# Optimization experiments

Measured on AMD Instinct MI355X. Metric: run time of the kernel, lower is better.

Reference implementation:

```python
import jax, jax.numpy as jnp
import numpy as np

N = 100000

def _gcn_layer(x, W, b, src, dst, norm):
    # dense transform then sparse normalized aggregation (scatter-add)
    h = x @ W                                  # [N, out]
    msg = h[src] * norm[:, None]               # [E+N, out]
    agg = jax.ops.segment_sum(msg, dst, num_segments=N)
    return agg + b


def setup_inputs() -> dict:
    key = jax.random.key(0)
    ks = jax.random.split(key, 12)
    num_features, hidden, num_classes = 128, 128, 32
    E = 3200000
    x = jax.random.normal(ks[0], (N, num_features), dtype=jnp.float32)
    edge_index = jax.random.randint(ks[1], (2, E), 0, N, dtype=jnp.int64)

    def glorot(k, fan_in, fan_out):
        s = (6.0 / (fan_in + fan_out)) ** 0.5
        return jax.random.uniform(k, (fan_in, fan_out), jnp.float32, -s, s)

    return {
        "x": x,
        "edge_index": edge_index,
        "W1": glorot(ks[2], num_features, hidden), "b1": jnp.zeros((hidden,), jnp.float32),
        "W2": glorot(ks[3], hidden, hidden),       "b2": jnp.zeros((hidden,), jnp.float32),
        "W3": glorot(ks[4], hidden, hidden),       "b3": jnp.zeros((hidden,), jnp.float32),
        "W4": glorot(ks[5], hidden, num_classes),  "b4": jnp.zeros((num_classes,), jnp.float32),
    }


def reference(x, edge_index, W1, b1, W2, b2, W3, b3, W4, b4):
    # GCNConv semantics: add self-loops, symmetric degree normalization
    loop = jnp.arange(N, dtype=edge_index.dtype)
    src = jnp.concatenate([edge_index[0], loop])   # [E+N]
    dst = jnp.concatenate([edge_index[1], loop])   # [E+N]
    deg = jax.ops.segment_sum(jnp.ones_like(dst, dtype=x.dtype), dst, num_segments=N)
    dinv = jnp.where(deg > 0, deg ** -0.5, 0.0)
    norm = dinv[src] * dinv[dst]                   # [E+N]

    h = _gcn_layer(x, W1, b1, src, dst, norm)
    h = jax.nn.relu(h)                              # dropout: eval mode -> identity
    h = _gcn_layer(h, W2, b2, src, dst, norm)
    h = jax.nn.relu(h)
    h = _gcn_layer(h, W3, b3, src, dst, norm)
    h = jax.nn.relu(h)
    h = _gcn_layer(h, W4, b4, src, dst, norm)
    return jax.nn.log_softmax(h, axis=1)
```

## Files before the change

### kernel.cpp

```cpp
#include <hip/hip_runtime.h>
#include <hip/hip_bf16.h>
#include <math.h>

#define NNODES 100000
#define NBMAX 512
#define CH 8192

typedef __hip_bfloat16 bf16;
typedef __attribute__((ext_vector_type(8))) short short8;
typedef __attribute__((ext_vector_type(4))) float f32x4;
typedef __attribute__((ext_vector_type(2))) float f32x2;

__device__ inline unsigned pack_bf16x2(float a, float b) {
    __hip_bfloat162 p;
    p.x = __float2bfloat16(a);
    p.y = __float2bfloat16(b);
    return *(unsigned*)&p;
}

__device__ inline float2 unpack_bf16x2(unsigned u) {
    __hip_bfloat162 p = *(__hip_bfloat162*)&u;
    return make_float2(__bfloat162float(p.x), __bfloat162float(p.y));
}

__device__ inline unsigned char f32_to_fp8(float v) {
    int p = __builtin_amdgcn_cvt_pk_fp8_f32(v, v, 0, false);
    return (unsigned char)(p & 0xff);
}

__global__ __launch_bounds__(256) void prep_w_all(const float* __restrict__ W1, bf16* __restrict__ wt1,
                                                  const float* __restrict__ W2, bf16* __restrict__ wt2,
                                                  const float* __restrict__ W3, bf16* __restrict__ wt3,
                                                  const float* __restrict__ W4, bf16* __restrict__ wt4,
                                                  int* __restrict__ bcount, int* __restrict__ done,
                                                  unsigned* __restrict__ zrow) {
    int b = blockIdx.x, t = threadIdx.x;
    if (b == 0) {
        for (int i = t; i < NBMAX; i += 256) bcount[i] = 0;
        if (t == 0) *done = 0;
        if (t < 32) zrow[t] = 0u;
    }
    const float* W; bf16* WT; int Nout, idx0;
    if (b < 64)       { W = W1; WT = wt1; Nout = 128; idx0 = b * 256; }
    else if (b < 128) { W = W2; WT = wt2; Nout = 128; idx0 = (b - 64) * 256; }
    else if (b < 192) { W = W3; WT = wt3; Nout = 128; idx0 = (b - 128) * 256; }
    else              { W = W4; WT = wt4; Nout = 32;  idx0 = (b - 192) * 256; }
    int idx = idx0 + t;
    if (idx < 128 * Nout) {
        int nn = idx >> 7;
        int kk = idx & 127;
        WT[idx] = __float2bfloat16(W[kk * Nout + nn]);
    }
}

__global__ __launch_bounds__(256) void bucket_hist_scan(const int* __restrict__ dst,
                                                        int* __restrict__ bcount,
                                                        int* __restrict__ boff,
                                                        int* __restrict__ bcursor,
                                                        int* __restrict__ done,
                                                        int E, int nb, int nblocks) {
    __shared__ int hist[NBMAX];
    __shared__ int ticket_s;
    __shared__ int wsum[4];
    int t = threadIdx.x;
    for (int i = t; i < NBMAX; i += 256) hist[i] = 0;
    __syncthreads();
    int e0 = blockIdx.x * CH;
#pragma unroll
    for (int k = 0; k < 32; ++k) {
        int e = e0 + t + k * 256;
        if (e < E) atomicAdd(&hist[dst[e] >> 8], 1);
    }
    __syncthreads();
    for (int i = t; i < nb; i += 256)
        if (hist[i]) atomicAdd(&bcount[i], hist[i]);
    __threadfence();
    __syncthreads();
    if (t == 0) ticket_s = atomicAdd(done, 1);
    __syncthreads();
    if (ticket_s != nblocks - 1) return;
    __threadfence();
    int i0 = t * 2, i1v = t * 2 + 1;
    int a  = (i0  < nb) ? atomicAdd(&bcount[i0], 0) : 0;
    int bb = (i1v < nb) ? atomicAdd(&bcount[i1v], 0) : 0;
    int v = a + bb;
    int lane = t & 63, wv = t >> 6;
    int incl = v;
#pragma unroll
    for (int dd = 1; dd < 64; dd <<= 1) {
        int x = __shfl_up(incl, dd, 64);
        if (lane >= dd) incl += x;
    }
    if (lane == 63) wsum[wv] = incl;
    __syncthreads();
    int wo = 0;
    for (int k = 0; k < wv; ++k) wo += wsum[k];
    int excl = wo + incl - v;
    if (i0 <= nb)  { boff[i0]  = excl;     if (i0  < nb) bcursor[i0]  = excl; }
    if (i1v <= nb) { boff[i1v] = excl + a; if (i1v < nb) bcursor[i1v] = excl + a; }
}

__global__ __launch_bounds__(256) void partition(const int* __restrict__ src,
                                                 const int* __restrict__ dst,
                                                 int* __restrict__ bcursor,
                                                 int* __restrict__ part, int E, int nb) {
    __shared__ int hist[NBMAX];
    __shared__ int cursor[NBMAX];
    int t = threadIdx.x;
    int e0 = blockIdx.x * CH;
    for (int i = t; i < NBMAX; i += 256) hist[i] = 0;
    __syncthreads();
    int mys[32], myd[32];
#pragma unroll
    for (int k = 0; k < 32; ++k) {
        int e = e0 + t + k * 256;
        int s = 0, dd = -1;
        if (e < E) { s = src[e]; dd = dst[e]; }
        mys[k] = s; myd[k] = dd;
        if (dd >= 0) atomicAdd(&hist[dd >> 8], 1);
    }
    __syncthreads();
    for (int i = t; i < nb; i += 256) {
        int c = hist[i];
        cursor[i] = c ? atomicAdd(&bcursor[i], c) : 0;
    }
    __syncthreads();
#pragma unroll
    for (int k = 0; k < 32; ++k) {
        int dd = myd[k];
        if (dd >= 0) {
            int lpos = atomicAdd(&cursor[dd >> 8], 1);
            part[lpos] = mys[k] | ((dd & 255) << 24);
        }
    }
}

__global__ __launch_bounds__(256) void nodes_fill(const int* __restrict__ part,
                                                  const int* __restrict__ boff,
                                                  float* __restrict__ dinv,
                                                  int2* __restrict__ off2,
                                                  int* __restrict__ edges, int n) {
    __shared__ int ndeg[256];
    __shared__ int ws2[4];
    __shared__ int offl[256];
    int b = blockIdx.x;
    int t = threadIdx.x;
    ndeg[t] = 0;
    __syncthreads();
    int r0 = boff[b], r1 = boff[b + 1];
    for (int i = r0 + t; i < r1; i += 256)
        atomicAdd(&ndeg[((unsigned)part[i]) >> 24], 1);
    __syncthreads();
    int deg = ndeg[t];
    int node = b * 256 + t;
    int lane = t & 63, wv = t >> 6;
    int incl = deg;
#pragma unroll
    for (int d = 1; d < 64; d <<= 1) {
        int x = __shfl_up(incl, d, 64);
        if (lane >= d) incl += x;
    }
    if (lane == 63) ws2[wv] = incl;
    __syncthreads();
    int wo = 0;
    for (int k = 0; k < wv; ++k) wo += ws2[k];
    int node_off = r0 + wo + incl - deg;
    if (node < n) {
        off2[node] = make_int2(node_off, node_off + deg);
        dinv[node] = rsqrtf((float)(deg + 1));
    }
    offl[t] = node_off;
    ndeg[t] = 0;
    __syncthreads();
    for (int i = r0 + t; i < r1; i += 256) {
        int rec = part[i];
        int dloc = ((unsigned)rec) >> 24;
        int lpos = atomicAdd(&ndeg[dloc], 1);
        edges[offl[dloc] + lpos] = rec & 0xFFFFFF;
    }
}

#define WSTRIDE 136

__global__ __launch_bounds__(256) void gemm128_f32A(const float* __restrict__ A,
                                                    const bf16* __restrict__ WT,
                                                    const float* __restrict__ dinv,
                                                    unsigned char* __restrict__ C, int n) {
    __shared__ bf16 wl[128 * WSTRIDE];
    int t = threadIdx.x;
#pragma unroll
    for (int l = 0; l < 8; ++l) {
        int chunk = t + l * 256;
        int row = chunk >> 4, ch = chunk & 15;
        *(uint4*)&wl[row * WSTRIDE + ch * 8] = *(const uint4*)&WT[row * 128 + ch * 8];
    }
    __syncthreads();
    int wave = t >> 6, lane = t & 63;
    int m = lane & 15, q = lane >> 4;
    int row_base = blockIdx.x * 128 + wave * 32;
    int r0 = min(row_base + m, n - 1);
    int r1 = min(row_base + 16 + m, n - 1);

    f32x4 acc[2][8];
#pragma unroll
    for (int g = 0; g < 2; ++g)
#pragma unroll
        for (int c = 0; c < 8; ++c) acc[g][c] = (f32x4)(0.f);

#pragma unroll
    for (int kt = 0; kt < 4; ++kt) {
        short8 af[2];
#pragma unroll
        for (int g = 0; g < 2; ++g) {
            const float* ap = &A[(size_t)(g ? r1 : r0) * 128 + kt * 32 + q * 8];
            float4 f0 = *(const float4*)ap;
            float4 f1 = *(const float4*)(ap + 4);
            union { uint4 u; short8 s; } cv;
            cv.u.x = pack_bf16x2(f0.x, f0.y);
            cv.u.y = pack_bf16x2(f0.z, f0.w);
            cv.u.z = pack_bf16x2(f1.x, f1.y);
            cv.u.w = pack_bf16x2(f1.z, f1.w);
            af[g] = cv.s;
        }
#pragma unroll
        for (int c = 0; c < 8; ++c) {
            short8 bf = *(const short8*)&wl[(c * 16 + m) * WSTRIDE + kt * 32 + q * 8];
            acc[0][c] = __builtin_amdgcn_mfma_f32_16x16x32_bf16(af[0], bf, acc[0][c], 0, 0, 0);
            acc[1][c] = __builtin_amdgcn_mfma_f32_16x16x32_bf16(af[1], bf, acc[1][c], 0, 0, 0);
        }
    }
    float dv[2][4];
#pragma unroll
    for (int g = 0; g < 2; ++g)
#pragma unroll
        for (int r = 0; r < 4; ++r) {
            int row = row_base + g * 16 + q * 4 + r;
            dv[g][r] = (row < n) ? dinv[row] : 0.f;
        }
#pragma unroll
    for (int g = 0; g < 2; ++g)
#pragma unroll
        for (int c = 0; c < 8; ++c)
#pragma unroll
            for (int r = 0; r < 4; ++r) {
                int row = row_base + g * 16 + q * 4 + r;
                if (row < n) C[(size_t)row * 128 + c * 16 + m] = f32_to_fp8(acc[g][c][r] * dv[g][r]);
            }
}

__global__ __launch_bounds__(256) void gemm128_bf16A(const bf16* __restrict__ A,
                                                     const bf16* __restrict__ WT,
                                                     const float* __restrict__ dinv,
                                                     unsigned char* __restrict__ C, int n) {
    __shared__ bf16 wl[128 * WSTRIDE];
    int t = threadIdx.x;
#pragma unroll
    for (int l = 0; l < 8; ++l) {
        int chunk = t + l * 256;
        int row = chunk >> 4, ch = chunk & 15;
        *(uint4*)&wl[row * WSTRIDE + ch * 8] = *(const uint4*)&WT[row * 128 + ch * 8];
    }
    __syncthreads();
    int wave = t >> 6, lane = t & 63;
    int m = lane & 15, q = lane >> 4;
    int row_base = blockIdx.x * 128 + wave * 32;
    int r0 = min(row_base + m, n - 1);
    int r1 = min(row_base + 16 + m, n - 1);

    f32x4 acc[2][8];
#pragma unroll
    for (int g = 0; g < 2; ++g)
#pragma unroll
        for (int c = 0; c < 8; ++c) acc[g][c] = (f32x4)(0.f);

#pragma unroll
    for (int kt = 0; kt < 4; ++kt) {
        short8 a0 = *(const short8*)&A[(size_t)r0 * 128 + kt * 32 + q * 8];
        short8 a1 = *(const short8*)&A[(size_t)r1 * 128 + kt * 32 + q * 8];
#pragma unroll
        for (int c = 0; c < 8; ++c) {
            short8 bf = *(const short8*)&wl[(c * 16 + m) * WSTRIDE + kt * 32 + q * 8];
            acc[0][c] = __builtin_amdgcn_mfma_f32_16x16x32_bf16(a0, bf, acc[0][c], 0, 0, 0);
            acc[1][c] = __builtin_amdgcn_mfma_f32_16x16x32_bf16(a1, bf, acc[1][c], 0, 0, 0);
        }
    }
    float dv[2][4];
#pragma unroll
    for (int g = 0; g < 2; ++g)
#pragma unroll
        for (int r = 0; r < 4; ++r) {
            int row = row_base + g * 16 + q * 4 + r;
            dv[g][r] = (row < n) ? dinv[row] : 0.f;
        }
#pragma unroll
    for (int g = 0; g < 2; ++g)
#pragma unroll
        for (int c = 0; c < 8; ++c)
#pragma unroll
            for (int r = 0; r < 4; ++r) {
                int row = row_base + g * 16 + q * 4 + r;
                if (row < n) C[(size_t)row * 128 + c * 16 + m] = f32_to_fp8(acc[g][c][r] * dv[g][r]);
            }
}

__global__ __launch_bounds__(256) void gemm32_bf16A(const bf16* __restrict__ A,
                                                    const bf16* __restrict__ WT,
                                                    const float* __restrict__ dinv,
                                                    bf16* __restrict__ C, int n) {
    if (blockIdx.x == 0 && threadIdx.x < 32)
        C[(size_t)n * 32 + threadIdx.x] = __float2bfloat16(0.f);
    int wave = threadIdx.x >> 6;
    int lane = threadIdx.x & 63;
    int m = lane & 15;
    int q = lane >> 4;
    int row_base = blockIdx.x * 64 + wave * 16;
    int arow = min(row_base + m, n - 1);

    f32x4 acc[2];
    acc[0] = (f32x4)(0.f);
    acc[1] = (f32x4)(0.f);

#pragma unroll
    for (int kt = 0; kt < 4; ++kt) {
        short8 af = *(const short8*)&A[(size_t)arow * 128 + kt * 32 + q * 8];
#pragma unroll
        for (int c = 0; c < 2; ++c) {
            short8 bf = *(const short8*)&WT[(size_t)(c * 16 + m) * 128 + kt * 32 + q * 8];
            acc[c] = __builtin_amdgcn_mfma_f32_16x16x32_bf16(af, bf, acc[c], 0, 0, 0);
        }
    }
    float dv[4];
#pragma unroll
    for (int r = 0; r < 4; ++r) {
        int row = row_base + q * 4 + r;
        dv[r] = (row < n) ? dinv[row] : 0.f;
    }
#pragma unroll
    for (int c = 0; c < 2; ++c)
#pragma unroll
        for (int r = 0; r < 4; ++r) {
            int row = row_base + q * 4 + r;
            if (row < n) C[(size_t)row * 32 + c * 16 + m] = __float2bfloat16(acc[c][r] * dv[r]);
        }
}

__global__ __launch_bounds__(256) void agg128(const unsigned char* __restrict__ h,
                                              const int2* __restrict__ off2,
                                              const int* __restrict__ edges,
                                              const float* __restrict__ dinv,
                                              const float* __restrict__ bias,
                                              bf16* __restrict__ out, int n) {
    int wid = (blockIdx.x * blockDim.x + threadIdx.x) >> 6;
    if (wid >= n) return;
    int lane = threadIdx.x & 63;
    int g = lane >> 4;
    int d = lane & 15;
    int l32 = lane & 31;
    const char* hb = (const char*)h;
    unsigned doff = (unsigned)(d << 3);

    int2 rng = off2[wid];
    int i0 = rng.x, i1 = rng.y;
    int deg = i1 - i0;
    int rem = deg & 31;
    int tail = i1 - rem;

    int tw = n;
    if (rem) {
        int te = edges[tail + l32];
        tw = (l32 < rem) ? te : n;
    }

    f32x2 A0 = {0.f, 0.f}, A1 = {0.f, 0.f}, A2 = {0.f, 0.f}, A3 = {0.f, 0.f};
    {
        uint2 su = *(const uint2*)(hb + (((unsigned)wid << 7) | doff));
        if (g) { su.x = 0u; su.y = 0u; }
        A0 += __builtin_amdgcn_cvt_pk_f32_fp8((int)su.x, false);
        A1 += __builtin_amdgcn_cvt_pk_f32_fp8((int)su.x, true);
        A2 += __builtin_amdgcn_cvt_pk_f32_fp8((int)su.y, false);
        A3 += __builtin_amdgcn_cvt_pk_f32_fp8((int)su.y, true);
    }

    int i = i0;
    int ew;
    if (i + 32 <= i1) ew = edges[i + l32];
    while (i + 32 <= i1) {
        int idxs[8];
#pragma unroll
        for (int j = 0; j < 8; ++j) idxs[j] = __shfl(ew, j * 4 + g, 64);
        uint2 uu[8];
#pragma unroll
        for (int j = 0; j < 8; ++j)
            uu[j] = *(const uint2*)(hb + (((unsigned)idxs[j] << 7) | doff));
        int inext = i + 32;
        if (inext + 32 <= i1) ew = edges[inext + l32];
#pragma unroll
        for (int j = 0; j < 8; ++j) {
            A0 += __builtin_amdgcn_cvt_pk_f32_fp8((int)uu[j].x, false);
            A1 += __builtin_amdgcn_cvt_pk_f32_fp8((int)uu[j].x, true);
            A2 += __builtin_amdgcn_cvt_pk_f32_fp8((int)uu[j].y, false);
            A3 += __builtin_amdgcn_cvt_pk_f32_fp8((int)uu[j].y, true);
        }
        i = inext;
    }
    if (rem) {
        int njg = (rem + 3) >> 2;
        int idxs[8];
        uint2 uu[8];
#pragma unroll
        for (int j = 0; j < 8; ++j)
            if (j < njg) idxs[j] = __shfl(tw, j * 4 + g, 64);
#pragma unroll
        for (int j = 0; j < 8; ++j)
            if (j < njg) uu[j] = *(const uint2*)(hb + (((unsigned)idxs[j] << 7) | doff));
#pragma unroll
        for (int j = 0; j < 8; ++j) {
            if (j < njg) {
                A0 += __builtin_amdgcn_cvt_pk_f32_fp8((int)uu[j].x, false);
                A1 += __builtin_amdgcn_cvt_pk_f32_fp8((int)uu[j].x, true);
                A2 += __builtin_amdgcn_cvt_pk_f32_fp8((int)uu[j].y, false);
                A3 += __builtin_amdgcn_cvt_pk_f32_fp8((int)uu[j].y, true);
            }
        }
    }
    float r0 = A0[0], r1 = A0[1], r2 = A1[0], r3 = A1[1];
    float r4 = A2[0], r5 = A2[1], r6 = A3[0], r7 = A3[1];
    r0 += __shfl_xor(r0, 16); r1 += __shfl_xor(r1, 16);
    r2 += __shfl_xor(r2, 16); r3 += __shfl_xor(r3, 16);
    r4 += __shfl_xor(r4, 16); r5 += __shfl_xor(r5, 16);
    r6 += __shfl_xor(r6, 16); r7 += __shfl_xor(r7, 16);
    r0 += __shfl_xor(r0, 32); r1 += __shfl_xor(r1, 32);
    r2 += __shfl_xor(r2, 32); r3 += __shfl_xor(r3, 32);
    r4 += __shfl_xor(r4, 32); r5 += __shfl_xor(r5, 32);
    r6 += __shfl_xor(r6, 32); r7 += __shfl_xor(r7, 32);
    float pa = (g & 1) ? r2 : r0;
    float pb = (g & 1) ? r3 : r1;
    float qa = (g & 1) ? r6 : r4;
    float qb = (g & 1) ? r7 : r5;
    pa = (g & 2) ? qa : pa;
    pb = (g & 2) ? qb : pb;

    float dl = dinv[wid];
    int od = d * 4 + g;
    float2 bv = *(const float2*)&bias[od * 2];
    float a0 = fmaxf(pa * dl + bv.x, 0.f);
    float a1 = fmaxf(pb * dl + bv.y, 0.f);
    ((unsigned*)out)[(size_t)wid * 64 + od] = pack_bf16x2(a0, a1);
}

__global__ __launch_bounds__(256) void agg32_lsm(const bf16* __restrict__ h,
                                                 const int2* __restrict__ off2,
                                                 const int* __restrict__ edges,
                                                 const float* __restrict__ dinv,
                                                 const float* __restrict__ bias,
                                                 float* __restrict__ out, int n) {
    int idx = blockIdx.x * blockDim.x + threadIdx.x;
    int node = idx >> 5;
    if (node >= n) return;
    int lane = threadIdx.x & 63;
    int halfbase = lane & 32;
    int lane5 = lane & 31;
    int g = lane5 >> 3;
    int d = lane5 & 7;
    int l16 = lane5 & 15;
    const char* hb = (const char*)h;
    unsigned doff = (unsigned)(d << 3);

    int2 rng = off2[node];
    int i0 = rng.x, i1 = rng.y;
    int deg = i1 - i0;
    int rem = deg & 15;
    int tail = i1 - rem;

    int tw = n;
    if (rem) {
        int te = edges[tail + l16];
        tw = (l16 < rem) ? te : n;
    }

    f32x2 acc0 = {0.f, 0.f}, acc1 = {0.f, 0.f};
    {
        uint2 su = *(const uint2*)(hb + (((unsigned)node << 6) | doff));
        if (g) { su.x = 0u; su.y = 0u; }
        float2 f0 = unpack_bf16x2(su.x), f1 = unpack_bf16x2(su.y);
        acc0[0] += f0.x; acc0[1] += f0.y; acc1[0] += f1.x; acc1[1] += f1.y;
    }
    int i = i0;
    int ew;
    if (i + 16 <= i1) ew = edges[i + l16];
    while (i + 16 <= i1) {
        int idxs[4];
#pragma unroll
        for (int j = 0; j < 4; ++j) idxs[j] = __shfl(ew, halfbase + j * 4 + g, 64);
        uint2 uu[4];
#pragma unroll
        for (int j = 0; j < 4; ++j)
            uu[j] = *(const uint2*)(hb + (((unsigned)idxs[j] << 6) | doff));
        int inext = i + 16;
        if (inext + 16 <= i1) ew = edges[inext + l16];
#pragma unroll
        for (int j = 0; j < 4; ++j) {
            float2 f0 = unpack_bf16x2(uu[j].x), f1 = unpack_bf16x2(uu[j].y);
            acc0[0] += f0.x; acc0[1] += f0.y; acc1[0] += f1.x; acc1[1] += f1.y;
        }
        i = inext;
    }
    if (rem) {
        int njg = (rem + 3) >> 2;
        int idxs[4];
        uint2 uu[4];
#pragma unroll
        for (int j = 0; j < 4; ++j)
            if (j < njg) idxs[j] = __shfl(tw, halfbase + j * 4 + g, 64);
#pragma unroll
        for (int j = 0; j < 4; ++j)
            if (j < njg) uu[j] = *(const uint2*)(hb + (((unsigned)idxs[j] << 6) | doff));
#pragma unroll
        for (int j = 0; j < 4; ++j) {
            if (j < njg) {
                float2 f0 = unpack_bf16x2(uu[j].x), f1 = unpack_bf16x2(uu[j].y);
                acc0[0] += f0.x; acc0[1] += f0.y; acc1[0] += f1.x; acc1[1] += f1.y;
            }
        }
    }
    float s0 = acc0[0], s1 = acc0[1], s2 = acc1[0], s3 = acc1[1];
    s0 += __shfl_xor(s0, 8);  s1 += __shfl_xor(s1, 8);
    s2 += __shfl_xor(s2, 8);  s3 += __shfl_xor(s3, 8);
    s0 += __shfl_xor(s0, 16); s1 += __shfl_xor(s1, 16);
    s2 += __shfl_xor(s2, 16); s3 += __shfl_xor(s3, 16);

    float dl = dinv[node];
    float4 bv = *(const float4*)&bias[d * 4];
    float a0 = s0 * dl + bv.x;
    float a1 = s1 * dl + bv.y;
    float a2 = s2 * dl + bv.z;
    float a3 = s3 * dl + bv.w;
    float m = fmaxf(fmaxf(a0, a1), fmaxf(a2, a3));
    for (int dd = 1; dd < 8; dd <<= 1) m = fmaxf(m, __shfl_xor(m, dd));
    float e = expf(a0 - m) + expf(a1 - m) + expf(a2 - m) + expf(a3 - m);
    for (int dd = 1; dd < 8; dd <<= 1) e += __shfl_xor(e, dd);
    float lse = m + logf(e);
    if (g == 0)
        *(float4*)&out[(size_t)node * 32 + d * 4] =
            make_float4(a0 - lse, a1 - lse, a2 - lse, a3 - lse);
}

extern "C" void kernel_launch(void* const* d_in, const int* in_sizes, int n_in,
                              void* d_out, int out_size, void* d_ws, size_t ws_size,
                              hipStream_t stream) {
    const float* x  = (const float*)d_in[0];
    const int*   ei = (const int*)d_in[1];
    const float* W1 = (const float*)d_in[2];
    const float* b1 = (const float*)d_in[3];
    const float* W2 = (const float*)d_in[4];
    const float* b2 = (const float*)d_in[5];
    const float* W3 = (const float*)d_in[6];
    const float* b3 = (const float*)d_in[7];
    const float* W4 = (const float*)d_in[8];
    const float* b4 = (const float*)d_in[9];
    float* out = (float*)d_out;

    const int N = NNODES;
    const int E = in_sizes[1] / 2;
    const int nb = (N + 255) / 256;

    char* ws = (char*)d_ws;
    size_t o = 0;
    auto alloc = [&](size_t bytes) -> void* {
        void* p = ws + o;
        o += (bytes + 255) & ~(size_t)255;
        return p;
    };
    int*   bcount  = (int*)alloc((size_t)NBMAX * 4);
    int*   boff    = (int*)alloc((size_t)(NBMAX + 1) * 4);
    int*   bcursor = (int*)alloc((size_t)NBMAX * 4);
    int*   done    = (int*)alloc(4);
    int2*  off2    = (int2*)alloc((size_t)N * 8);
    float* dinv    = (float*)alloc((size_t)N * 4);
    int*   part    = (int*)alloc((size_t)E * 8);
    int*   edges   = (int*)alloc((size_t)(E + 64) * 4);
    bf16*  wt1     = (bf16*)alloc((size_t)128 * 128 * 2);
    bf16*  wt2     = (bf16*)alloc((size_t)128 * 128 * 2);
    bf16*  wt3     = (bf16*)alloc((size_t)128 * 128 * 2);
    bf16*  wt4     = (bf16*)alloc((size_t)32 * 128 * 2);
    unsigned char* hbuf = (unsigned char*)alloc((size_t)(N + 1) * 128);
    bf16*  gbuf    = (bf16*)part;

    const int* srcv = ei;
    const int* dstv = ei + E;

    int pblocks = (E + CH - 1) / CH;

    prep_w_all<<<208, 256, 0, stream>>>(W1, wt1, W2, wt2, W3, wt3, W4, wt4,
                                        bcount, done, (unsigned*)(hbuf + (size_t)N * 128));
    bucket_hist_scan<<<pblocks, 256, 0, stream>>>(dstv, bcount, boff, bcursor, done,
                                                  E, nb, pblocks);
    partition<<<pblocks, 256, 0, stream>>>(srcv, dstv, bcursor, part, E, nb);
    nodes_fill<<<nb, 256, 0, stream>>>(part, boff, dinv, off2, edges, N);

    int gemm128_blocks = (N + 127) / 128;
    int gemm32_blocks = (N + 63) / 64;
    int agg128_blocks = (N + 3) / 4;
    int agg32_blocks = (N * 32 + 255) / 256;

    gemm128_f32A<<<gemm128_blocks, 256, 0, stream>>>(x, wt1, dinv, hbuf, N);
    agg128<<<agg128_blocks, 256, 0, stream>>>(hbuf, off2, edges, dinv, b1, gbuf, N);
    gemm128_bf16A<<<gemm128_blocks, 256, 0, stream>>>(gbuf, wt2, dinv, hbuf, N);
    agg128<<<agg128_blocks, 256, 0, stream>>>(hbuf, off2, edges, dinv, b2, gbuf, N);
    gemm128_bf16A<<<gemm128_blocks, 256, 0, stream>>>(gbuf, wt3, dinv, hbuf, N);
    agg128<<<agg128_blocks, 256, 0, stream>>>(hbuf, off2, edges, dinv, b3, gbuf, N);
    gemm32_bf16A<<<gemm32_blocks, 256, 0, stream>>>(gbuf, wt4, dinv, (bf16*)hbuf, N);
    agg32_lsm<<<agg32_blocks, 256, 0, stream>>>((const bf16*)hbuf, off2, edges, dinv, b4, out, N);
}
```

Baseline: 470.9 us.

## Build CSR with global per-node atomics and widen agg128 gathers to 16B

Replaces the two-pass bucket partition CSR build with a per-node degree count using global atomics, a bucket-sum and scan, per-node offsets, and a direct atomic-cursor fill of the edges array. This drops the intermediate packed partition buffer and its second pass. The cost is heavy global atomic contention on 3.2M edges and a nondeterministic edge order within each node. The agg128 kernel now has 8 lanes per row loading 16 bytes each instead of 16 lanes loading 8 bytes, with a butterfly transpose-reduce across lanes. That halves gather instructions at the cost of more registers.

```diff
diff --git a/kernel.cpp b/kernel.cpp
--- a/kernel.cpp
+++ b/kernel.cpp
@@ -32,14 +32,11 @@
                                                   const float* __restrict__ W2, bf16* __restrict__ wt2,
                                                   const float* __restrict__ W3, bf16* __restrict__ wt3,
                                                   const float* __restrict__ W4, bf16* __restrict__ wt4,
-                                                  int* __restrict__ bcount, int* __restrict__ done,
+                                                  int* __restrict__ deg,
                                                   unsigned* __restrict__ zrow) {
     int b = blockIdx.x, t = threadIdx.x;
-    if (b == 0) {
-        for (int i = t; i < NBMAX; i += 256) bcount[i] = 0;
-        if (t == 0) *done = 0;
-        if (t < 32) zrow[t] = 0u;
-    }
+    for (int i = b * 256 + t; i < NNODES; i += 208 * 256) deg[i] = 0;
+    if (b == 0 && t < 32) zrow[t] = 0u;
     const float* W; bf16* WT; int Nout, idx0;
     if (b < 64)       { W = W1; WT = wt1; Nout = 128; idx0 = b * 256; }
     else if (b < 128) { W = W2; WT = wt2; Nout = 128; idx0 = (b - 64) * 256; }
@@ -53,108 +50,59 @@
     }
 }
 
-__global__ __launch_bounds__(256) void bucket_hist_scan(const int* __restrict__ dst,
-                                                        int* __restrict__ bcount,
-                                                        int* __restrict__ boff,
-                                                        int* __restrict__ bcursor,
-                                                        int* __restrict__ done,
-                                                        int E, int nb, int nblocks) {
-    __shared__ int hist[NBMAX];
-    __shared__ int ticket_s;
-    __shared__ int wsum[4];
+__global__ __launch_bounds__(256) void deg_count(const int* __restrict__ dst,
+                                                 int* __restrict__ deg, int E) {
+    int e0 = blockIdx.x * CH + threadIdx.x;
+#pragma unroll
+    for (int k = 0; k < 32; ++k) {
+        int e = e0 + k * 256;
+        if (e < E) atomicAdd(&deg[dst[e]], 1);
+    }
+}
+
+__global__ __launch_bounds__(256) void bucket_sums(const int* __restrict__ deg,
+                                                   int* __restrict__ bsum, int n) {
+    __shared__ int ws[4];
+    int b = blockIdx.x, t = threadIdx.x;
+    int node = b * 256 + t;
+    int v = (node < n) ? deg[node] : 0;
+#pragma unroll
+    for (int m = 1; m < 64; m <<= 1) v += __shfl_xor(v, m, 64);
+    if ((t & 63) == 0) ws[t >> 6] = v;
+    __syncthreads();
+    if (t == 0) bsum[b] = ws[0] + ws[1] + ws[2] + ws[3];
+}
+
+__global__ __launch_bounds__(512) void bucket_scan(const int* __restrict__ bsum,
+                                                   int* __restrict__ bbase, int nb) {
+    __shared__ int wsum[8];
     int t = threadIdx.x;
-    for (int i = t; i < NBMAX; i += 256) hist[i] = 0;
-    __syncthreads();
-    int e0 = blockIdx.x * CH;
-#pragma unroll
-    for (int k = 0; k < 32; ++k) {
-        int e = e0 + t + k * 256;
-        if (e < E) atomicAdd(&hist[dst[e] >> 8], 1);
-    }
-    __syncthreads();
-    for (int i = t; i < nb; i += 256)
-        if (hist[i]) atomicAdd(&bcount[i], hist[i]);
-    __threadfence();
-    __syncthreads();
-    if (t == 0) ticket_s = atomicAdd(done, 1);
-    __syncthreads();
-    if (ticket_s != nblocks - 1) return;
-    __threadfence();
-    int i0 = t * 2, i1v = t * 2 + 1;
-    int a  = (i0  < nb) ? atomicAdd(&bcount[i0], 0) : 0;
-    int bb = (i1v < nb) ? atomicAdd(&bcount[i1v], 0) : 0;
-    int v = a + bb;
+    int v = (t < nb) ? bsum[t] : 0;
     int lane = t & 63, wv = t >> 6;
     int incl = v;
 #pragma unroll
-    for (int dd = 1; dd < 64; dd <<= 1) {
-        int x = __shfl_up(incl, dd, 64);
-        if (lane >= dd) incl += x;
+    for (int d = 1; d < 64; d <<= 1) {
+        int x = __shfl_up(incl, d, 64);
+        if (lane >= d) incl += x;
     }
     if (lane == 63) wsum[wv] = incl;
     __syncthreads();
     int wo = 0;
     for (int k = 0; k < wv; ++k) wo += wsum[k];
-    int excl = wo + incl - v;
-    if (i0 <= nb)  { boff[i0]  = excl;     if (i0  < nb) bcursor[i0]  = excl; }
-    if (i1v <= nb) { boff[i1v] = excl + a; if (i1v < nb) bcursor[i1v] = excl + a; }
-}
-
-__global__ __launch_bounds__(256) void partition(const int* __restrict__ src,
-                                                 const int* __restrict__ dst,
-                                                 int* __restrict__ bcursor,
-                                                 int* __restrict__ part, int E, int nb) {
-    __shared__ int hist[NBMAX];
-    __shared__ int cursor[NBMAX];
-    int t = threadIdx.x;
-    int e0 = blockIdx.x * CH;
-    for (int i = t; i < NBMAX; i += 256) hist[i] = 0;
-    __syncthreads();
-    int mys[32], myd[32];
-#pragma unroll
-    for (int k = 0; k < 32; ++k) {
-        int e = e0 + t + k * 256;
-        int s = 0, dd = -1;
-        if (e < E) { s = src[e]; dd = dst[e]; }
-        mys[k] = s; myd[k] = dd;
-        if (dd >= 0) atomicAdd(&hist[dd >> 8], 1);
-    }
-    __syncthreads();
-    for (int i = t; i < nb; i += 256) {
-        int c = hist[i];
-        cursor[i] = c ? atomicAdd(&bcursor[i], c) : 0;
-    }
-    __syncthreads();
-#pragma unroll
-    for (int k = 0; k < 32; ++k) {
-        int dd = myd[k];
-        if (dd >= 0) {
-            int lpos = atomicAdd(&cursor[dd >> 8], 1);
-            part[lpos] = mys[k] | ((dd & 255) << 24);
-        }
-    }
-}
-
-__global__ __launch_bounds__(256) void nodes_fill(const int* __restrict__ part,
-                                                  const int* __restrict__ boff,
-                                                  float* __restrict__ dinv,
+    if (t <= nb) bbase[t] = wo + incl - v;
+}
+
+__global__ __launch_bounds__(256) void node_off_k(const int* __restrict__ deg,
+                                                  const int* __restrict__ bbase,
                                                   int2* __restrict__ off2,
-                                                  int* __restrict__ edges, int n) {
-    __shared__ int ndeg[256];
+                                                  int* __restrict__ cursor,
+                                                  float* __restrict__ dinv, int n) {
     __shared__ int ws2[4];
-    __shared__ int offl[256];
-    int b = blockIdx.x;
-    int t = threadIdx.x;
-    ndeg[t] = 0;
-    __syncthreads();
-    int r0 = boff[b], r1 = boff[b + 1];
-    for (int i = r0 + t; i < r1; i += 256)
-        atomicAdd(&ndeg[((unsigned)part[i]) >> 24], 1);
-    __syncthreads();
-    int deg = ndeg[t];
+    int b = blockIdx.x, t = threadIdx.x;
     int node = b * 256 + t;
+    int v = (node < n) ? deg[node] : 0;
     int lane = t & 63, wv = t >> 6;
-    int incl = deg;
+    int incl = v;
 #pragma unroll
     for (int d = 1; d < 64; d <<= 1) {
         int x = __shfl_up(incl, d, 64);
@@ -164,19 +112,27 @@
     __syncthreads();
     int wo = 0;
     for (int k = 0; k < wv; ++k) wo += ws2[k];
-    int node_off = r0 + wo + incl - deg;
+    int off = bbase[b] + wo + incl - v;
     if (node < n) {
-        off2[node] = make_int2(node_off, node_off + deg);
-        dinv[node] = rsqrtf((float)(deg + 1));
-    }
-    offl[t] = node_off;
-    ndeg[t] = 0;
-    __syncthreads();
-    for (int i = r0 + t; i < r1; i += 256) {
-        int rec = part[i];
-        int dloc = ((unsigned)rec) >> 24;
-        int lpos = atomicAdd(&ndeg[dloc], 1);
-        edges[offl[dloc] + lpos] = rec & 0xFFFFFF;
+        off2[node] = make_int2(off, off + v);
+        cursor[node] = off;
+        dinv[node] = rsqrtf((float)(v + 1));
+    }
+}
+
+__global__ __launch_bounds__(256) void csr_fill(const int* __restrict__ src,
+                                                const int* __restrict__ dst,
+                                                int* __restrict__ cursor,
+                                                int* __restrict__ edges, int E) {
+    int e0 = blockIdx.x * CH + threadIdx.x;
+#pragma unroll
+    for (int k = 0; k < 32; ++k) {
+        int e = e0 + k * 256;
+        if (e < E) {
+            int s = src[e], d = dst[e];
+            int pos = atomicAdd(&cursor[d], 1);
+            edges[pos] = s;
+        }
     }
 }
 
@@ -353,11 +309,11 @@
     int wid = (blockIdx.x * blockDim.x + threadIdx.x) >> 6;
     if (wid >= n) return;
     int lane = threadIdx.x & 63;
-    int g = lane >> 4;
-    int d = lane & 15;
+    int g = lane >> 3;
+    int d = lane & 7;
     int l32 = lane & 31;
     const char* hb = (const char*)h;
-    unsigned doff = (unsigned)(d << 3);
+    unsigned doff = (unsigned)(d << 4);
 
     int2 rng = off2[wid];
     int i0 = rng.x, i1 = rng.y;
@@ -371,80 +327,99 @@
         tw = (l32 < rem) ? te : n;
     }
 
-    f32x2 A0 = {0.f, 0.f}, A1 = {0.f, 0.f}, A2 = {0.f, 0.f}, A3 = {0.f, 0.f};
-    {
-        uint2 su = *(const uint2*)(hb + (((unsigned)wid << 7) | doff));
-        if (g) { su.x = 0u; su.y = 0u; }
-        A0 += __builtin_amdgcn_cvt_pk_f32_fp8((int)su.x, false);
-        A1 += __builtin_amdgcn_cvt_pk_f32_fp8((int)su.x, true);
-        A2 += __builtin_amdgcn_cvt_pk_f32_fp8((int)su.y, false);
-        A3 += __builtin_amdgcn_cvt_pk_f32_fp8((int)su.y, true);
+    f32x2 A[8];
+#pragma unroll
+    for (int q = 0; q < 8; ++q) A[q] = (f32x2){0.f, 0.f};
+
+    if (g == 0) {
+        uint4 su = *(const uint4*)(hb + (((unsigned)wid << 7) | doff));
+        A[0] += __builtin_amdgcn_cvt_pk_f32_fp8((int)su.x, false);
+        A[1] += __builtin_amdgcn_cvt_pk_f32_fp8((int)su.x, true);
+        A[2] += __builtin_amdgcn_cvt_pk_f32_fp8((int)su.y, false);
+        A[3] += __builtin_amdgcn_cvt_pk_f32_fp8((int)su.y, true);
+        A[4] += __builtin_amdgcn_cvt_pk_f32_fp8((int)su.z, false);
+        A[5] += __builtin_amdgcn_cvt_pk_f32_fp8((int)su.z, true);
+        A[6] += __builtin_amdgcn_cvt_pk_f32_fp8((int)su.w, false);
+        A[7] += __builtin_amdgcn_cvt_pk_f32_fp8((int)su.w, true);
     }
 
     int i = i0;
     int ew;
     if (i + 32 <= i1) ew = edges[i + l32];
     while (i + 32 <= i1) {
-        int idxs[8];
-#pragma unroll
-        for (int j = 0; j < 8; ++j) idxs[j] = __shfl(ew, j * 4 + g, 64);
-        uint2 uu[8];
-#pragma unroll
-        for (int j = 0; j < 8; ++j)
-            uu[j] = *(const uint2*)(hb + (((unsigned)idxs[j] << 7) | doff));
+        int idxs[4];
+#pragma unroll
+        for (int j = 0; j < 4; ++j) idxs[j] = __shfl(ew, j * 8 + g, 64);
+        uint4 uu[4];
+#pragma unroll
+        for (int j = 0; j < 4; ++j)
+            uu[j] = *(const uint4*)(hb + (((unsigned)idxs[j] << 7) | doff));
         int inext = i + 32;
         if (inext + 32 <= i1) ew = edges[inext + l32];
 #pragma unroll
-        for (int j = 0; j < 8; ++j) {
-            A0 += __builtin_amdgcn_cvt_pk_f32_fp8((int)uu[j].x, false);
-            A1 += __builtin_amdgcn_cvt_pk_f32_fp8((int)uu[j].x, true);
-            A2 += __builtin_amdgcn_cvt_pk_f32_fp8((int)uu[j].y, false);
-            A3 += __builtin_amdgcn_cvt_pk_f32_fp8((int)uu[j].y, true);
+        for (int j = 0; j < 4; ++j) {
+            A[0] += __builtin_amdgcn_cvt_pk_f32_fp8((int)uu[j].x, false);
+            A[1] += __builtin_amdgcn_cvt_pk_f32_fp8((int)uu[j].x, true);
+            A[2] += __builtin_amdgcn_cvt_pk_f32_fp8((int)uu[j].y, false);
+            A[3] += __builtin_amdgcn_cvt_pk_f32_fp8((int)uu[j].y, true);
+            A[4] += __builtin_amdgcn_cvt_pk_f32_fp8((int)uu[j].z, false);
+            A[5] += __builtin_amdgcn_cvt_pk_f32_fp8((int)uu[j].z, true);
+            A[6] += __builtin_amdgcn_cvt_pk_f32_fp8((int)uu[j].w, false);
+            A[7] += __builtin_amdgcn_cvt_pk_f32_fp8((int)uu[j].w, true);
         }
         i = inext;
     }
     if (rem) {
-        int njg = (rem + 3) >> 2;
-        int idxs[8];
-        uint2 uu[8];
-#pragma unroll
-        for (int j = 0; j < 8; ++j)
-            if (j < njg) idxs[j] = __shfl(tw, j * 4 + g, 64);
-#pragma unroll
-        for (int j = 0; j < 8; ++j)
-            if (j < njg) uu[j] = *(const uint2*)(hb + (((unsigned)idxs[j] << 7) | doff));
-#pragma unroll
-        for (int j = 0; j < 8; ++j) {
+        int njg = (rem + 7) >> 3;
+        int idxs[4];
+        uint4 uu[4];
+#pragma unroll
+        for (int j = 0; j < 4; ++j)
+            if (j < njg) idxs[j] = __shfl(tw, j * 8 + g, 64);
+#pragma unroll
+        for (int j = 0; j < 4; ++j)
+            if (j < njg) uu[j] = *(const uint4*)(hb + (((unsigned)idxs[j] << 7) | doff));
+#pragma unroll
+        for (int j = 0; j < 4; ++j) {
             if (j < njg) {
-                A0 += __builtin_amdgcn_cvt_pk_f32_fp8((int)uu[j].x, false);
-                A1 += __builtin_amdgcn_cvt_pk_f32_fp8((int)uu[j].x, true);
-                A2 += __builtin_amdgcn_cvt_pk_f32_fp8((int)uu[j].y, false);
-                A3 += __builtin_amdgcn_cvt_pk_f32_fp8((int)uu[j].y, true);
+                A[0] += __builtin_amdgcn_cvt_pk_f32_fp8((int)uu[j].x, false);
+                A[1] += __builtin_amdgcn_cvt_pk_f32_fp8((int)uu[j].x, true);
+                A[2] += __builtin_amdgcn_cvt_pk_f32_fp8((int)uu[j].y, false);
+                A[3] += __builtin_amdgcn_cvt_pk_f32_fp8((int)uu[j].y, true);
+                A[4] += __builtin_amdgcn_cvt_pk_f32_fp8((int)uu[j].z, false);
+                A[5] += __builtin_amdgcn_cvt_pk_f32_fp8((int)uu[j].z, true);
+                A[6] += __builtin_amdgcn_cvt_pk_f32_fp8((int)uu[j].w, false);
+                A[7] += __builtin_amdgcn_cvt_pk_f32_fp8((int)uu[j].w, true);
             }
         }
     }
-    float r0 = A0[0], r1 = A0[1], r2 = A1[0], r3 = A1[1];
-    float r4 = A2[0], r5 = A2[1], r6 = A3[0], r7 = A3[1];
-    r0 += __shfl_xor(r0, 16); r1 += __shfl_xor(r1, 16);
-    r2 += __shfl_xor(r2, 16); r3 += __shfl_xor(r3, 16);
-    r4 += __shfl_xor(r4, 16); r5 += __shfl_xor(r5, 16);
-    r6 += __shfl_xor(r6, 16); r7 += __shfl_xor(r7, 16);
-    r0 += __shfl_xor(r0, 32); r1 += __shfl_xor(r1, 32);
-    r2 += __shfl_xor(r2, 32); r3 += __shfl_xor(r3, 32);
-    r4 += __shfl_xor(r4, 32); r5 += __shfl_xor(r5, 32);
-    r6 += __shfl_xor(r6, 32); r7 += __shfl_xor(r7, 32);
-    float pa = (g & 1) ? r2 : r0;
-    float pb = (g & 1) ? r3 : r1;
-    float qa = (g & 1) ? r6 : r4;
-    float qb = (g & 1) ? r7 : r5;
-    pa = (g & 2) ? qa : pa;
-    pb = (g & 2) ? qb : pb;
-
+    bool k0 = (g & 1) != 0, k1 = (g & 2) != 0, k2 = (g & 4) != 0;
+    f32x2 B1[4];
+#pragma unroll
+    for (int q = 0; q < 4; ++q) {
+        f32x2 K = k0 ? A[q + 4] : A[q];
+        f32x2 S = k0 ? A[q] : A[q + 4];
+        f32x2 R; R[0] = __shfl_xor(S[0], 8, 64); R[1] = __shfl_xor(S[1], 8, 64);
+        B1[q] = K + R;
+    }
+    f32x2 B2[2];
+#pragma unroll
+    for (int q = 0; q < 2; ++q) {
+        f32x2 K = k1 ? B1[q + 2] : B1[q];
+        f32x2 S = k1 ? B1[q] : B1[q + 2];
+        f32x2 R; R[0] = __shfl_xor(S[0], 16, 64); R[1] = __shfl_xor(S[1], 16, 64);
+        B2[q] = K + R;
+    }
+    f32x2 K3 = k2 ? B2[1] : B2[0];
+    f32x2 S3 = k2 ? B2[0] : B2[1];
+    f32x2 R3; R3[0] = __shfl_xor(S3[0], 32, 64); R3[1] = __shfl_xor(S3[1], 32, 64);
+    f32x2 F = K3 + R3;
+
+    int od = d * 8 + (k0 ? 4 : 0) + (k1 ? 2 : 0) + (k2 ? 1 : 0);
     float dl = dinv[wid];
-    int od = d * 4 + g;
     float2 bv = *(const float2*)&bias[od * 2];
-    float a0 = fmaxf(pa * dl + bv.x, 0.f);
-    float a1 = fmaxf(pb * dl + bv.y, 0.f);
+    float a0 = fmaxf(F[0] * dl + bv.x, 0.f);
+    float a1 = fmaxf(F[1] * dl + bv.y, 0.f);
     ((unsigned*)out)[(size_t)wid * 64 + od] = pack_bf16x2(a0, a1);
 }
 
@@ -571,20 +546,19 @@
         o += (bytes + 255) & ~(size_t)255;
         return p;
     };
-    int*   bcount  = (int*)alloc((size_t)NBMAX * 4);
-    int*   boff    = (int*)alloc((size_t)(NBMAX + 1) * 4);
-    int*   bcursor = (int*)alloc((size_t)NBMAX * 4);
-    int*   done    = (int*)alloc(4);
+    int*   deg     = (int*)alloc((size_t)N * 4);
+    int*   cursor  = (int*)alloc((size_t)N * 4);
+    int*   bsum    = (int*)alloc((size_t)(NBMAX + 1) * 4);
+    int*   bbase   = (int*)alloc((size_t)(NBMAX + 1) * 4);
     int2*  off2    = (int2*)alloc((size_t)N * 8);
     float* dinv    = (float*)alloc((size_t)N * 4);
-    int*   part    = (int*)alloc((size_t)E * 8);
+    bf16*  gbuf    = (bf16*)alloc((size_t)N * 128 * 2);
     int*   edges   = (int*)alloc((size_t)(E + 64) * 4);
     bf16*  wt1     = (bf16*)alloc((size_t)128 * 128 * 2);
     bf16*  wt2     = (bf16*)alloc((size_t)128 * 128 * 2);
     bf16*  wt3     = (bf16*)alloc((size_t)128 * 128 * 2);
     bf16*  wt4     = (bf16*)alloc((size_t)32 * 128 * 2);
     unsigned char* hbuf = (unsigned char*)alloc((size_t)(N + 1) * 128);
-    bf16*  gbuf    = (bf16*)part;
 
     const int* srcv = ei;
     const int* dstv = ei + E;
@@ -592,11 +566,12 @@
     int pblocks = (E + CH - 1) / CH;
 
     prep_w_all<<<208, 256, 0, stream>>>(W1, wt1, W2, wt2, W3, wt3, W4, wt4,
-                                        bcount, done, (unsigned*)(hbuf + (size_t)N * 128));
-    bucket_hist_scan<<<pblocks, 256, 0, stream>>>(dstv, bcount, boff, bcursor, done,
-                                                  E, nb, pblocks);
-    partition<<<pblocks, 256, 0, stream>>>(srcv, dstv, bcursor, part, E, nb);
-    nodes_fill<<<nb, 256, 0, stream>>>(part, boff, dinv, off2, edges, N);
+                                        deg, (unsigned*)(hbuf + (size_t)N * 128));
+    deg_count<<<pblocks, 256, 0, stream>>>(dstv, deg, E);
+    bucket_sums<<<nb, 256, 0, stream>>>(deg, bsum, N);
+    bucket_scan<<<1, 512, 0, stream>>>(bsum, bbase, nb);
+    node_off_k<<<nb, 256, 0, stream>>>(deg, bbase, off2, cursor, dinv, N);
+    csr_fill<<<pblocks, 256, 0, stream>>>(srcv, dstv, cursor, edges, E);
 
     int gemm128_blocks = (N + 127) / 128;
     int gemm32_blocks = (N + 63) / 64;
```

Result: slower. 773.4 us (+64.2%).
